# Optimization experiments

Measured on AMD Instinct MI355X. Metric: run time of the kernel, lower is better.

Reference implementation:

```python
import jax, jax.numpy as jnp
import numpy as np

THRESH = 0.9   # config['thresh_cnn']
R = 2          # config['radius'] -> maxpool kernel 2R+1=5, stride 1, padding R


def setup_inputs() -> dict:
    key = jax.random.key(0)
    # [B=1, C=1, D=64, H=512, W=512]
    pred_vol = jax.random.uniform(key, (1, 1, 64, 512, 512), dtype=jnp.float32)
    return {"pred_vol": pred_vol}


def reference(pred_vol):
    # threshold: keep values > thresh, else 0
    pred_thresh = jnp.where(pred_vol > THRESH, pred_vol, 0.0)
    # 3D max-pool, kernel 2R+1, stride 1, padding R (torch pads with -inf for maxpool)
    k = 2 * R + 1
    mp = jax.lax.reduce_window(
        pred_thresh, -jnp.inf, jax.lax.max,
        window_dimensions=(1, 1, k, k, k),
        window_strides=(1, 1, 1, 1, 1),
        padding=[(0, 0), (0, 0), (R, R), (R, R), (R, R)],
    )
    # keep only strict local maxima of the thresholded volume
    conf_vol = jnp.where((mp > 0.0) & (mp == pred_thresh), mp, 0.0)
    return jnp.squeeze(conf_vol)  # [D, H, W] dense peak confidence map
```

## Files before the change

kernel.cpp:

```cpp
#include <hip/hip_runtime.h>


#define THRESH 0.9f

constexpr int D = 64, H = 512, W = 512;
constexpr int HW = H * W;
constexpr int TW = 64;
constexpr int TH = 16;
constexpr int DCHUNK = 8;
constexpr int HALO = 2;
constexpr int LROWS = TH + 2 * HALO;
constexpr int WM_S = 17;
constexpr int NS = DCHUNK + 2 * HALO;

typedef float floatx4 __attribute__((ext_vector_type(4)));
typedef float floatx2 __attribute__((ext_vector_type(2)));

__device__ __forceinline__ void barrier_no_drain() {
    asm volatile("s_waitcnt lgkmcnt(0)\n\ts_barrier" ::: "memory");
}

__device__ __forceinline__ float4 max4(float4 a, float4 b) {
    return make_float4(fmaxf(a.x, b.x), fmaxf(a.y, b.y),
                       fmaxf(a.z, b.z), fmaxf(a.w, b.w));
}

__device__ __forceinline__ float4 wmax5s(floatx2 l, float4 b, floatx2 r) {
    const float f2 = l.x, f3 = l.y, f4 = b.x, f5 = b.y, f6 = b.z, f7 = b.w;
    const float f8 = r.x, f9 = r.y;
    const float m45 = fmaxf(f4, f5);
    const float m56 = fmaxf(f5, f6);
    const float m345 = fmaxf(f3, m45);
    const float m456 = fmaxf(f4, m56);
    const float m567 = fmaxf(m56, f7);
    const float m678 = fmaxf(fmaxf(f6, f7), f8);
    float4 q;
    q.x = fmaxf(fmaxf(f2, f6), m345);
    q.y = fmaxf(fmaxf(f3, f7), m456);
    q.z = fmaxf(fmaxf(f4, f8), m567);
    q.w = fmaxf(fmaxf(f5, f9), m678);
    return q;
}

__global__ __launch_bounds__(320)
void peak3d_kernel(const float* __restrict__ in, float* __restrict__ out) {
    __shared__ float4 wm[2][LROWS * WM_S];

    const int tx = threadIdx.x;
    const int ty = threadIdx.y;

    const int w0 = blockIdx.x * TW;
    const int h0 = blockIdx.y * TH;
    const int d0 = blockIdx.z * DCHUNK;

    const int gh  = h0 + ty - HALO;
    const bool vR = (unsigned)gh < (unsigned)H;
    const int gwm = w0 + 4 * tx;
    const bool vl = vR && (gwm >= 2);
    const bool vr = vR && (gwm + 4 < W);
    const unsigned rbase = (unsigned)(vR ? gh : 0) * W;
    const unsigned offm = rbase + (unsigned)gwm;
    const unsigned ocen = (unsigned)(h0 + ty) * W + (unsigned)gwm;

    const float4 zero4 = make_float4(0.f, 0.f, 0.f, 0.f);
    const floatx2 zero2 = {0.f, 0.f};
    float4 win[5];
#pragma unroll
    for (int k = 0; k < 5; ++k) win[k] = zero4;
    float4 cen_pf = zero4;

    auto loadStage = [&](int dd, float4& m, floatx2& l, floatx2& r) {
        m = zero4; l = zero2; r = zero2;
        if (dd >= 0 && dd < D) {
            const float* sb = in + (size_t)dd * HW;
            if (vR) m = *reinterpret_cast<const float4*>(sb + offm);
            if (vl) l = *reinterpret_cast<const floatx2*>(sb + offm - 2);
            if (vr) r = *reinterpret_cast<const floatx2*>(sb + offm + 4);
        }
    };

    float4 pm; floatx2 pl, pr;
    loadStage(d0 - HALO, pm, pl, pr);

#pragma unroll
    for (int t = 0; t < NS; ++t) {
        const int buf = t & 1;

        wm[buf][ty * WM_S + tx] = wmax5s(pl, pm, pr);

        if (t >= 4 && ty < TH)
            cen_pf = *reinterpret_cast<const float4*>(
                in + (size_t)(d0 + (t - 4)) * HW + ocen);

        if (t + 1 < NS) loadStage(d0 - HALO + t + 1, pm, pl, pr);

        barrier_no_drain();

        if (ty < TH) {
            const float4* wp = &wm[buf][ty * WM_S + tx];
            const float4 hv = max4(max4(max4(wp[0 * WM_S], wp[1 * WM_S]),
                                        max4(wp[3 * WM_S], wp[4 * WM_S])),
                                   wp[2 * WM_S]);
            win[t % 5] = hv;

            if (t >= 4) {
                const int dout = d0 + (t - 4);
                const float4 mp = max4(max4(max4(win[0], win[1]),
                                            max4(win[2], win[3])), win[4]);
                const float4 c = cen_pf;
                floatx4 res;
                res.x = (c.x > THRESH && mp.x == c.x) ? c.x : 0.f;
                res.y = (c.y > THRESH && mp.y == c.y) ? c.y : 0.f;
                res.z = (c.z > THRESH && mp.z == c.z) ? c.z : 0.f;
                res.w = (c.w > THRESH && mp.w == c.w) ? c.w : 0.f;
                floatx4* op = reinterpret_cast<floatx4*>(
                    out + (size_t)dout * HW + ocen);
                __builtin_nontemporal_store(res, op);
            }
        }
    }
}

extern "C" void kernel_launch(void* const* d_in, const int* in_sizes, int n_in,
                              void* d_out, int out_size, void* d_ws, size_t ws_size,
                              hipStream_t stream) {
    const float* in = (const float*)d_in[0];
    float* out = (float*)d_out;
    dim3 grid(W / TW, H / TH, D / DCHUNK);
    dim3 block(16, LROWS, 1);
    hipLaunchKernelGGL(peak3d_kernel, grid, block, 0, stream, in, out);
}
```

Before: 123.1 us.

## Double depth chunk and process two depth stages per barrier

Increases the depth chunk per block from 8 to 16 slices, reducing redundant halo slice reads. The loop now handles two depth stages per iteration with four shared-memory buffers, halving barriers and prefetching two stages ahead. The cost is fewer blocks in flight and higher register use.

```diff
diff --git a/kernel.cpp b/kernel.cpp
--- a/kernel.cpp
+++ b/kernel.cpp
@@ -7,11 +7,12 @@
 constexpr int HW = H * W;
 constexpr int TW = 64;
 constexpr int TH = 16;
-constexpr int DCHUNK = 8;
+constexpr int DCHUNK = 16;
 constexpr int HALO = 2;
 constexpr int LROWS = TH + 2 * HALO;
 constexpr int WM_S = 17;
 constexpr int NS = DCHUNK + 2 * HALO;
+constexpr int NPAIR = NS / 2;
 
 typedef float floatx4 __attribute__((ext_vector_type(4)));
 typedef float floatx2 __attribute__((ext_vector_type(2)));
@@ -44,7 +45,7 @@
 
 __global__ __launch_bounds__(320)
 void peak3d_kernel(const float* __restrict__ in, float* __restrict__ out) {
-    __shared__ float4 wm[2][LROWS * WM_S];
+    __shared__ float4 wm[4][LROWS * WM_S];
 
     const int tx = threadIdx.x;
     const int ty = threadIdx.y;
@@ -67,10 +68,11 @@
     float4 win[5];
 #pragma unroll
     for (int k = 0; k < 5; ++k) win[k] = zero4;
-    float4 cen_pf = zero4;
+    float4 cen0 = zero4, cen1 = zero4;
 
-    auto loadStage = [&](int dd, float4& m, floatx2& l, floatx2& r) {
+    auto loadStage = [&](int s, float4& m, floatx2& l, floatx2& r) {
         m = zero4; l = zero2; r = zero2;
+        const int dd = d0 - HALO + s;
         if (dd >= 0 && dd < D) {
             const float* sb = in + (size_t)dd * HW;
             if (vR) m = *reinterpret_cast<const float4*>(sb + offm);
@@ -79,43 +81,71 @@
         }
     };
 
-    float4 pm; floatx2 pl, pr;
-    loadStage(d0 - HALO, pm, pl, pr);
+    float4 pm0, pm1; floatx2 pl0, pr0, pl1, pr1;
+    loadStage(0, pm0, pl0, pr0);
+    loadStage(1, pm1, pl1, pr1);
 
 #pragma unroll
-    for (int t = 0; t < NS; ++t) {
-        const int buf = t & 1;
+    for (int i = 0; i < NPAIR; ++i) {
+        const int s0 = 2 * i, s1 = 2 * i + 1;
 
-        wm[buf][ty * WM_S + tx] = wmax5s(pl, pm, pr);
+        wm[s0 & 3][ty * WM_S + tx] = wmax5s(pl0, pm0, pr0);
+        wm[s1 & 3][ty * WM_S + tx] = wmax5s(pl1, pm1, pr1);
 
-        if (t >= 4 && ty < TH)
-            cen_pf = *reinterpret_cast<const float4*>(
-                in + (size_t)(d0 + (t - 4)) * HW + ocen);
+        if (i >= 2 && ty < TH) {
+            cen0 = *reinterpret_cast<const float4*>(
+                in + (size_t)(d0 + (2 * i - 4)) * HW + ocen);
+            cen1 = *reinterpret_cast<const float4*>(
+                in + (size_t)(d0 + (2 * i - 3)) * HW + ocen);
+        }
 
-        if (t + 1 < NS) loadStage(d0 - HALO + t + 1, pm, pl, pr);
+        if (i + 1 < NPAIR) {
+            loadStage(s0 + 2, pm0, pl0, pr0);
+            loadStage(s1 + 2, pm1, pl1, pr1);
+        }
 
         barrier_no_drain();
 
         if (ty < TH) {
-            const float4* wp = &wm[buf][ty * WM_S + tx];
-            const float4 hv = max4(max4(max4(wp[0 * WM_S], wp[1 * WM_S]),
-                                        max4(wp[3 * WM_S], wp[4 * WM_S])),
-                                   wp[2 * WM_S]);
-            win[t % 5] = hv;
-
-            if (t >= 4) {
-                const int dout = d0 + (t - 4);
+            {
+                const float4* wp = &wm[s0 & 3][ty * WM_S + tx];
+                const float4 hv = max4(max4(max4(wp[0 * WM_S], wp[1 * WM_S]),
+                                            max4(wp[3 * WM_S], wp[4 * WM_S])),
+                                       wp[2 * WM_S]);
+                win[s0 % 5] = hv;
+            }
+            if (i >= 2) {
+                const int dout = d0 + (2 * i - 4);
                 const float4 mp = max4(max4(max4(win[0], win[1]),
                                             max4(win[2], win[3])), win[4]);
-                const float4 c = cen_pf;
+                const float4 c = cen0;
                 floatx4 res;
                 res.x = (c.x > THRESH && mp.x == c.x) ? c.x : 0.f;
                 res.y = (c.y > THRESH && mp.y == c.y) ? c.y : 0.f;
                 res.z = (c.z > THRESH && mp.z == c.z) ? c.z : 0.f;
                 res.w = (c.w > THRESH && mp.w == c.w) ? c.w : 0.f;
-                floatx4* op = reinterpret_cast<floatx4*>(
-                    out + (size_t)dout * HW + ocen);
-                __builtin_nontemporal_store(res, op);
+                __builtin_nontemporal_store(res, reinterpret_cast<floatx4*>(
+                    out + (size_t)dout * HW + ocen));
+            }
+            {
+                const float4* wp = &wm[s1 & 3][ty * WM_S + tx];
+                const float4 hv = max4(max4(max4(wp[0 * WM_S], wp[1 * WM_S]),
+                                            max4(wp[3 * WM_S], wp[4 * WM_S])),
+                                       wp[2 * WM_S]);
+                win[s1 % 5] = hv;
+            }
+            if (i >= 2) {
+                const int dout = d0 + (2 * i - 3);
+                const float4 mp = max4(max4(max4(win[0], win[1]),
+                                            max4(win[2], win[3])), win[4]);
+                const float4 c = cen1;
+                floatx4 res;
+                res.x = (c.x > THRESH && mp.x == c.x) ? c.x : 0.f;
+                res.y = (c.y > THRESH && mp.y == c.y) ? c.y : 0.f;
+                res.z = (c.z > THRESH && mp.z == c.z) ? c.z : 0.f;
+                res.w = (c.w > THRESH && mp.w == c.w) ? c.w : 0.f;
+                __builtin_nontemporal_store(res, reinterpret_cast<floatx4*>(
+                    out + (size_t)dout * HW + ocen));
             }
         }
     }
```

After: 119.4 us. -3.1%, faster.
